# Performance work log

Hardware: AMD Instinct MI355X
Metric: run time of the kernel (lower is better)

## Reference

```python
import jax, jax.numpy as jnp
import numpy as np

N, E, MUL = 10000, 160000, 16
DIM = 9            # sum of 2l+1 for l=0..2
UV = 5             # 2*lmax+1
CONV = 9           # uv1 + uv2 - 1
ONE = CONV // 2 + 1
LOG2 = np.float32(np.log(2.0))


def _ssp(x):
    # ShiftedSoftPlus
    return jax.nn.softplus(x) - LOG2


def _build_a_w():
    # weight_align_matrix scaled by path_w ~ sqrt(2l+1): row l covers its (2l+1) block
    a = np.zeros((3, DIM), dtype=np.float32)
    off = 0
    for l in range(3):
        d = 2 * l + 1
        a[l, off:off + d] = np.sqrt(np.float32(d))
        off += d
    return jnp.asarray(a)


def setup_inputs() -> dict:
    key = jax.random.key(0)
    ks = jax.random.split(key, 14)
    inp = {
        "x": jax.random.normal(ks[0], (N, MUL, DIM), jnp.float32),
        "filter_sph": jax.random.normal(ks[1], (E, DIM), jnp.float32),
        "weight_in": jax.random.uniform(ks[2], (E, 8), jnp.float32),
        "edge_idx": jax.random.randint(ks[3], (2, E), 0, N),
        "Ux_re": jax.random.normal(ks[4], (DIM, UV, UV), jnp.float32),
        "Ux_im": jax.random.normal(ks[5], (DIM, UV, UV), jnp.float32),
        "Uf_re": jax.random.normal(ks[6], (DIM, UV, UV), jnp.float32),
        "Uf_im": jax.random.normal(ks[7], (DIM, UV, UV), jnp.float32),
        "Vout_re": jax.random.normal(ks[8], (CONV, ONE, DIM), jnp.float32),
        "Vout_im": jax.random.normal(ks[9], (CONV, ONE, DIM), jnp.float32),
        "W1": jax.random.normal(ks[10], (8, 64), jnp.float32),
        "W2": jax.random.normal(ks[11], (64, 64), jnp.float32),
        "W3": jax.random.normal(ks[12], (64, MUL * 3), jnp.float32),
        "a_w": _build_a_w(),
        "denominator": jnp.ones((1,), jnp.float32),
    }
    return inp


def _to_grid(coeff, U):
    # coeff [..., DIM] real; U [DIM, UV, UV] complex -> real grid [..., CONV, CONV]
    f = jnp.einsum('...d,duv->...uv', coeff.astype(U.dtype), U)
    pad = (CONV - UV) // 2
    cfg = [(0, 0)] * (f.ndim - 2) + [(pad, pad), (pad, pad)]
    fp = jnp.pad(f, cfg)
    fo = jnp.fft.ifftshift(fp, axes=(-2, -1))[..., :ONE]
    return jnp.fft.irfft2(fo, s=(CONV, CONV), axes=(-2, -1), norm='backward')


def reference(x, filter_sph, weight_in, edge_idx, Ux_re, Ux_im, Uf_re, Uf_im,
              Vout_re, Vout_im, W1, W2, W3, a_w, denominator):
    Ux = jax.lax.complex(Ux_re, Ux_im)
    Uf = jax.lax.complex(Uf_re, Uf_im)
    Vo = jax.lax.complex(Vout_re, Vout_im)
    edge_src = edge_idx[1]
    edge_dst = edge_idx[0]

    # node and filter signals on the CONVxCONV Fourier grid
    xf = _to_grid(x, Ux)                             # [N, MUL, 9, 9]
    yf = _to_grid(filter_sph[:, None, :], Uf)        # [E, 1, 9, 9]

    conv = xf[edge_src] * yf                         # [E, MUL, 9, 9]
    out_f = jnp.fft.rfft2(conv, axes=(-2, -1))       # [E, MUL, 9, 5] complex
    msg = jnp.einsum('emuv,uvd->emd', out_f, Vo).real  # ToSphericalBasis (hermitian input)

    # weight MLP (e3nn FullyConnectedNet: x @ W / sqrt(fan_in), ssp between)
    h = _ssp(weight_in @ W1 * (1.0 / np.sqrt(8.0, dtype=np.float32)))
    h = _ssp(h @ W2 * (1.0 / np.sqrt(64.0, dtype=np.float32)))
    w = (h @ W3 * (1.0 / np.sqrt(64.0, dtype=np.float32))).reshape(-1, MUL, 3)

    factor = jnp.einsum('emp,pd->emd', w, a_w)       # weight @ a_w
    message = msg * factor                           # [E, MUL, 9]

    out = jax.ops.segment_sum(message, edge_dst, num_segments=N)  # scatter-reduce sum
    return out / denominator[0]
```

## Files before the change

### kernel.cpp

```cpp
#include <hip/hip_runtime.h>
#include <math.h>

#define PI9 (2.0f * 3.14159265358979323846f / 9.0f)

typedef float f32x4 __attribute__((ext_vector_type(4)));
typedef unsigned short us8 __attribute__((ext_vector_type(8)));
typedef __bf16 bf16x8 __attribute__((ext_vector_type(8)));
typedef unsigned int u32x4 __attribute__((ext_vector_type(4)));

__device__ __forceinline__ float ssp_f(float x) {
  const float ax = fabsf(x);
  const float t = __expf(-ax);
  return fmaxf(x, 0.f) + __logf(1.f + t) - 0.69314718f;
}

__device__ __forceinline__ unsigned short f2bf(float f) {
  unsigned int u = __float_as_uint(f);
  unsigned int r = (u + 0x7FFFu + ((u >> 16) & 1u)) >> 16;
  return (unsigned short)r;
}

__device__ __forceinline__ float bfLO(unsigned int u) {
  return __uint_as_float(u << 16);
}
__device__ __forceinline__ float bfHI(unsigned int u) {
  return __uint_as_float(u & 0xffff0000u);
}

__global__ __launch_bounds__(256) void wconv_kernel(
    const float* __restrict__ W1, const float* __restrict__ W2,
    const float* __restrict__ W3, const float* __restrict__ a_w,
    const float* __restrict__ den, float* __restrict__ W1s,
    unsigned short* __restrict__ W2T, unsigned short* __restrict__ W3T) {
  const int i = blockIdx.x * 256 + threadIdx.x;
  const float invden = 1.f / den[0];
  const float sc0 = a_w[0] * invden, sc1 = a_w[10] * invden, sc2 = a_w[22] * invden;
  const float rs8 = 0.35355339059327373f;
  if (i < 512) {
    W1s[i] = W1[i] * rs8;
  } else if (i < 4608) {
    const int ii = i - 512;
    const int k = ii >> 6, j = ii & 63;
    W2T[j * 64 + ((((k >> 3) ^ (j & 7)) << 3)) + (k & 7)] = f2bf(W2[ii] * 0.125f);
  } else if (i < 7680) {
    const int ii = i - 4608;
    const int k = ii / 48, j = ii % 48;
    const int jm = j % 3;
    const float s = (jm == 0) ? sc0 : ((jm == 1) ? sc1 : sc2);
    W3T[j * 64 + ((((k >> 3) ^ (j & 7)) << 3)) + (k & 7)] = f2bf(W3[ii] * 0.125f * s);
  }
}

__device__ void precompute_body(
    int d, unsigned char* smem,
    const float* __restrict__ Ux_re, const float* __restrict__ Ux_im,
    const float* __restrict__ Uf_re, const float* __restrict__ Uf_im,
    const float* __restrict__ Vo_re, const float* __restrict__ Vo_im,
    float* __restrict__ CT) {
  float* G = (float*)smem;
  float* TL = (float*)(smem + 5840);
  float* cs9 = (float*)(smem + 8768);
  float* sn9 = (float*)(smem + 8816);
  const int t0 = threadIdx.x;

  if (t0 < 9) {
    float s, c;
    __sincosf(PI9 * (float)t0, &s, &c);
    cs9[t0] = c; sn9[t0] = s;
  }
  __syncthreads();

  for (int t = t0; t < 1458; t += 256) {
    const int which = t / 729, idx = t % 729;
    const int p = idx / 81, ab = idx % 81, a = ab / 9, b = ab % 9;
    const float* Ure = which ? Uf_re : Ux_re;
    const float* Uim = which ? Uf_im : Ux_im;
    float g = 0.f;
#pragma unroll
    for (int v = 0; v < 3; ++v) {
      const int uc = v + 2;
      float hre = 0.f, him = 0.f;
#pragma unroll
      for (int ui = 0; ui < 5; ++ui) {
        const int u = (ui + 7) % 9;
        const float re = Ure[p * 25 + ui * 5 + uc];
        const float im = Uim[p * 25 + ui * 5 + uc];
        const int k = (u * a) % 9;
        const float c = cs9[k], s = sn9[k];
        hre += re * c - im * s;
        him += re * s + im * c;
      }
      hre *= (1.f / 9.f); him *= (1.f / 9.f);
      if (v == 0) {
        g += hre;
      } else {
        const int k = (v * b) % 9;
        g += 2.f * (hre * cs9[k] - him * sn9[k]);
      }
    }
    G[which * 729 + p * 81 + ab] = g * (1.f / 9.f);
  }
  __syncthreads();

  for (int t = t0; t < 729; t += 256) {
    const int ab = t / 9, dd = t % 9, a = ab / 9, b = ab % 9;
    float acc = 0.f;
    for (int u = 0; u < 9; ++u)
      for (int v = 0; v < 5; ++v) {
        const int k = (u * a + v * b) % 9;
        acc += Vo_re[u * 45 + v * 9 + dd] * cs9[k]
             + Vo_im[u * 45 + v * 9 + dd] * sn9[k];
      }
    TL[ab * 9 + dd] = acc;
  }
  __syncthreads();

  if (t0 < 108) {
    const int p = t0 / 12, q = t0 % 12;
    float acc = 0.f;
    if (q < 9) {
      for (int ab = 0; ab < 81; ++ab)
        acc += G[p * 81 + ab] * G[729 + q * 81 + ab] * TL[ab * 9 + d];
    }
    CT[(d * 9 + p) * 12 + q] = acc;
  }
}

__device__ void mlp_body(
    int mblk, unsigned char* smem, const float* __restrict__ win,
    const float* __restrict__ W1s, const unsigned short* __restrict__ W2T,
    const unsigned short* __restrict__ W3T,
    unsigned short* __restrict__ w48b) {
  unsigned short* H1 = (unsigned short*)smem;
  unsigned short* H2 = (unsigned short*)(smem + 8192);
  const int t = threadIdx.x;
  const int w = t >> 6, l = t & 63;
  const int er = l & 15, g = l >> 4;
  unsigned short* h1p = H1 + w * 1024;
  unsigned short* h2p = H2 + w * 1024;

#pragma unroll 1
  for (int rep = 0; rep < 2; ++rep) {
    const int e = mblk * 128 + rep * 64 + w * 16 + er;

    float in8[8];
    {
      const float4 A = *(const float4*)(win + (size_t)e * 8);
      const float4 B = *(const float4*)(win + (size_t)e * 8 + 4);
      in8[0] = A.x; in8[1] = A.y; in8[2] = A.z; in8[3] = A.w;
      in8[4] = B.x; in8[5] = B.y; in8[6] = B.z; in8[7] = B.w;
    }
    float h[16];
#pragma unroll
    for (int c = 0; c < 16; ++c) h[c] = 0.f;
#pragma unroll
    for (int k = 0; k < 8; ++k) {
      const float* wr = W1s + k * 64 + g * 16;
      const float4 w0 = *(const float4*)wr;
      const float4 w1 = *(const float4*)(wr + 4);
      const float4 w2 = *(const float4*)(wr + 8);
      const float4 w3 = *(const float4*)(wr + 12);
      const float ik = in8[k];
      h[0]  = fmaf(ik, w0.x, h[0]);  h[1]  = fmaf(ik, w0.y, h[1]);
      h[2]  = fmaf(ik, w0.z, h[2]);  h[3]  = fmaf(ik, w0.w, h[3]);
      h[4]  = fmaf(ik, w1.x, h[4]);  h[5]  = fmaf(ik, w1.y, h[5]);
      h[6]  = fmaf(ik, w1.z, h[6]);  h[7]  = fmaf(ik, w1.w, h[7]);
      h[8]  = fmaf(ik, w2.x, h[8]);  h[9]  = fmaf(ik, w2.y, h[9]);
      h[10] = fmaf(ik, w2.z, h[10]); h[11] = fmaf(ik, w2.w, h[11]);
      h[12] = fmaf(ik, w3.x, h[12]); h[13] = fmaf(ik, w3.y, h[13]);
      h[14] = fmaf(ik, w3.z, h[14]); h[15] = fmaf(ik, w3.w, h[15]);
    }
    us8 pk0, pk1;
#pragma unroll
    for (int jj = 0; jj < 8; ++jj) pk0[jj] = f2bf(ssp_f(h[jj]));
#pragma unroll
    for (int jj = 0; jj < 8; ++jj) pk1[jj] = f2bf(ssp_f(h[8 + jj]));
    *(us8*)&h1p[er * 64 + (((2 * g) ^ (er & 7)) << 3)] = pk0;
    *(us8*)&h1p[er * 64 + (((2 * g + 1) ^ (er & 7)) << 3)] = pk1;
    __builtin_amdgcn_wave_barrier();

    const us8 a0 = *(const us8*)&h1p[er * 64 + ((g ^ (er & 7)) << 3)];
    const us8 a1 = *(const us8*)&h1p[er * 64 + (((g + 4) ^ (er & 7)) << 3)];
    float hh[16];
#pragma unroll
    for (int nt = 0; nt < 4; ++nt) {
      const int j = nt * 16 + er;
      const us8 b0 = *(const us8*)&W2T[j * 64 + ((g ^ (j & 7)) << 3)];
      const us8 b1 = *(const us8*)&W2T[j * 64 + (((g + 4) ^ (j & 7)) << 3)];
      f32x4 acc = {0.f, 0.f, 0.f, 0.f};
      acc = __builtin_amdgcn_mfma_f32_16x16x32_bf16(
          __builtin_bit_cast(bf16x8, a0), __builtin_bit_cast(bf16x8, b0), acc, 0, 0, 0);
      acc = __builtin_amdgcn_mfma_f32_16x16x32_bf16(
          __builtin_bit_cast(bf16x8, a1), __builtin_bit_cast(bf16x8, b1), acc, 0, 0, 0);
#pragma unroll
      for (int r = 0; r < 4; ++r) hh[nt * 4 + r] = ssp_f(acc[r]);
    }
#pragma unroll
    for (int nt = 0; nt < 4; ++nt)
#pragma unroll
      for (int r = 0; r < 4; ++r) {
        const int e2 = g * 4 + r;
        const int k2 = nt * 16 + er;
        h2p[e2 * 64 + ((((k2 >> 3) ^ (e2 & 7)) << 3)) + (k2 & 7)] = f2bf(hh[nt * 4 + r]);
      }
    __builtin_amdgcn_wave_barrier();

    const us8 c0 = *(const us8*)&h2p[er * 64 + ((g ^ (er & 7)) << 3)];
    const us8 c1 = *(const us8*)&h2p[er * 64 + (((g + 4) ^ (er & 7)) << 3)];
    const int ebase = mblk * 128 + rep * 64 + w * 16 + g * 4;
#pragma unroll
    for (int nt = 0; nt < 3; ++nt) {
      const int o = nt * 16 + er;
      const int om = o / 3, ol = o - om * 3;
      const us8 b0 = *(const us8*)&W3T[o * 64 + ((g ^ (o & 7)) << 3)];
      const us8 b1 = *(const us8*)&W3T[o * 64 + (((g + 4) ^ (o & 7)) << 3)];
      f32x4 acc = {0.f, 0.f, 0.f, 0.f};
      acc = __builtin_amdgcn_mfma_f32_16x16x32_bf16(
          __builtin_bit_cast(bf16x8, c0), __builtin_bit_cast(bf16x8, b0), acc, 0, 0, 0);
      acc = __builtin_amdgcn_mfma_f32_16x16x32_bf16(
          __builtin_bit_cast(bf16x8, c1), __builtin_bit_cast(bf16x8, b1), acc, 0, 0, 0);
#pragma unroll
      for (int r = 0; r < 4; ++r)
        w48b[(size_t)(ebase + r) * 64 + ol * 16 + om] = f2bf(acc[r]);
    }
    __builtin_amdgcn_wave_barrier();
  }
}

__global__ __launch_bounds__(256) void prep_kernel(
    const float* __restrict__ win, const float* __restrict__ W1s,
    const unsigned short* __restrict__ W2T,
    const unsigned short* __restrict__ W3T,
    unsigned short* __restrict__ w48b,
    const int* __restrict__ dst, const int* __restrict__ src, int E,
    int* __restrict__ cnt, int2* __restrict__ slots2,
    const float* __restrict__ xsrc, int NR, unsigned short* __restrict__ xbf,
    const float* __restrict__ Ux_re, const float* __restrict__ Ux_im,
    const float* __restrict__ Uf_re, const float* __restrict__ Uf_im,
    const float* __restrict__ Vo_re, const float* __restrict__ Vo_im,
    float* __restrict__ CT, int nScat, int nXc) {
  __shared__ __align__(16) unsigned char smem[16384];
  const int bid = blockIdx.x;
  if (bid < 9) {
    precompute_body(bid, smem, Ux_re, Ux_im, Uf_re, Uf_im, Vo_re, Vo_im, CT);
  } else if (bid < 9 + nScat) {
    const int e = (bid - 9) * 256 + threadIdx.x;
    if (e < E) {
      const int d = dst[e];
      const int pos = atomicAdd(&cnt[d], 1);
      if (pos < 96) slots2[(size_t)d * 96 + pos] = make_int2(e, src[e]);
    }
  } else if (bid < 9 + nScat + nXc) {
    const int r = (bid - 9 - nScat) * 256 + threadIdx.x;
    if (r < NR) {
      const float* xp = xsrc + (size_t)r * 9;
      unsigned int u0 = (unsigned)f2bf(xp[0]) | ((unsigned)f2bf(xp[1]) << 16);
      unsigned int u1 = (unsigned)f2bf(xp[2]) | ((unsigned)f2bf(xp[3]) << 16);
      unsigned int u2 = (unsigned)f2bf(xp[4]) | ((unsigned)f2bf(xp[5]) << 16);
      unsigned int u3 = (unsigned)f2bf(xp[6]) | ((unsigned)f2bf(xp[7]) << 16);
      unsigned int u4 = (unsigned)f2bf(xp[8]);
      unsigned short* op = xbf + (size_t)r * 12;
      *(uint2*)op = make_uint2(u0, u1);
      *(uint2*)(op + 4) = make_uint2(u2, u3);
      *(uint2*)(op + 8) = make_uint2(u4, 0u);
    }
  } else {
    mlp_body(bid - 9 - nScat - nXc, smem, win, W1s, W2T, W3T, w48b);
  }
}

__global__ __launch_bounds__(256) void node_kernel(
    const unsigned short* __restrict__ xbf, const float* __restrict__ filt,
    const int* __restrict__ cnt, const int2* __restrict__ slots2,
    const unsigned short* __restrict__ w48b, const float* __restrict__ CT,
    float* __restrict__ out, int N) {
  __shared__ __align__(16) unsigned short meL[4][2304];
  const int t = threadIdx.x, w = t >> 6, l = t & 63;
  const int n16 = l & 15, g = l >> 4;
  const int Ld = (n16 == 0) ? 0 : ((n16 < 4) ? 1 : 2);
  const bool dok = n16 < 9;
  const int drow = dok ? n16 : 0;
  const bool isg0 = (g == 0), isg1 = (g == 1);
  const int n = blockIdx.x * 4 + w;
  if (n >= N) return;

  int dT0, pT0, dT1, pT1, dT2, pT2, dT3, pT3, dT4, pT4, dT5, pT5;
  bool ok0, ok1, ok2, ok3, ok4, ok5;
  bf16x8 Bme0, Bme1, Bme2, Bme3, Bme4, Bme5;
#define MKB(tt, Bv, dv, pv, okv)                                             \
  {                                                                          \
    const int col = tt * 16 + n16;                                           \
    okv = (col < 81);                                                        \
    dv = okv ? col / 9 : 0;                                                  \
    pv = okv ? col % 9 : 0;                                                  \
    bf16x8 bv;                                                               \
    _Pragma("unroll")                                                        \
    for (int j = 0; j < 8; ++j) bv[j] = (__bf16)0.f;                         \
    if (okv) {                                                               \
      const float* cp = CT + col * 12;                                       \
      if (g == 0) {                                                          \
        const float4 ca = *(const float4*)cp;                                \
        const float4 cb = *(const float4*)(cp + 4);                          \
        bv[0] = (__bf16)ca.x; bv[1] = (__bf16)ca.y;                          \
        bv[2] = (__bf16)ca.z; bv[3] = (__bf16)ca.w;                          \
        bv[4] = (__bf16)cb.x; bv[5] = (__bf16)cb.y;                          \
        bv[6] = (__bf16)cb.z; bv[7] = (__bf16)cb.w;                          \
      } else if (g == 1) {                                                   \
        bv[0] = (__bf16)cp[8];                                               \
      }                                                                      \
    }                                                                        \
    Bv = bv;                                                                 \
  }
  MKB(0, Bme0, dT0, pT0, ok0); MKB(1, Bme1, dT1, pT1, ok1);
  MKB(2, Bme2, dT2, pT2, ok2); MKB(3, Bme3, dT3, pT3, ok3);
  MKB(4, Bme4, dT4, pT4, ok4); MKB(5, Bme5, dT5, pT5, ok5);
#undef MKB

  int deg = cnt[n];
  if (deg > 96) deg = 96;
  const int2* sl2 = slots2 + (size_t)n * 96;
  unsigned short* mlw = &meL[w][0];

  f32x4 accm = {0.f, 0.f, 0.f, 0.f};

  const int nb = (deg + 15) >> 4;
  for (int b = 0; b < nb; ++b) {
    const int base = b * 16;
    const int degb = (deg - base < 16) ? (deg - base) : 16;

    int esx = 0, esy = 0;
    if (n16 < degb) {
      const int2 v = sl2[base + n16];
      esx = v.x; esy = v.y;
    }
    bf16x8 Af;
#pragma unroll
    for (int j = 0; j < 8; ++j) Af[j] = (__bf16)0.f;
    if (n16 < degb) {
      const float* fp = filt + (size_t)esx * 9;
      if (g == 0) {
        const float4 fa = *(const float4*)fp;
        const float4 fb = *(const float4*)(fp + 4);
        Af[0] = (__bf16)fa.x; Af[1] = (__bf16)fa.y;
        Af[2] = (__bf16)fa.z; Af[3] = (__bf16)fa.w;
        Af[4] = (__bf16)fb.x; Af[5] = (__bf16)fb.y;
        Af[6] = (__bf16)fb.z; Af[7] = (__bf16)fb.w;
      } else if (g == 1) {
        Af[0] = (__bf16)fp[8];
      }
    }

#define MEMFMA(Bv, dv, pv, okv)                                              \
    {                                                                        \
      f32x4 a6 = {0.f, 0.f, 0.f, 0.f};                                       \
      a6 = __builtin_amdgcn_mfma_f32_16x16x32_bf16(Af, Bv, a6, 0, 0, 0);     \
      if (okv) {                                                             \
        _Pragma("unroll")                                                    \
        for (int r = 0; r < 4; ++r)                                          \
          mlw[(g * 4 + r) * 144 + dv * 16 + pv] = f2bf(a6[r]);               \
      }                                                                      \
    }
    MEMFMA(Bme0, dT0, pT0, ok0); MEMFMA(Bme1, dT1, pT1, ok1);
    MEMFMA(Bme2, dT2, pT2, ok2); MEMFMA(Bme3, dT3, pT3, ok3);
    MEMFMA(Bme4, dT4, pT4, ok4); MEMFMA(Bme5, dT5, pT5, ok5);
#undef MEMFMA
    __builtin_amdgcn_wave_barrier();

    for (int il = 0; il < degb; ++il) {
      const int e = __builtin_amdgcn_readlane(esx, il);
      const int s = __builtin_amdgcn_readlane(esy, il);

      const unsigned short* xrp = xbf + (size_t)s * 192 + n16 * 12;
      const u32x4 q = *(const u32x4*)xrp;
      const unsigned int qc = *(const unsigned int*)(xrp + 8);

      const uint2 wv =
          *(const uint2*)(w48b + (size_t)e * 64 + Ld * 16 + g * 4);

      const unsigned short* mr = mlw + il * 144 + drow * 16;
      const u32x4 mdv = *(const u32x4*)mr;
      const unsigned int md4 = (*(const unsigned int*)(mr + 8)) & 0xffffu;

      u32x4 av;
      av[0] = isg0 ? q[0] : (isg1 ? qc : 0u);
      av[1] = isg0 ? q[1] : 0u;
      av[2] = isg0 ? q[2] : 0u;
      av[3] = isg0 ? q[3] : 0u;
      u32x4 bv;
      bv[0] = isg0 ? mdv[0] : (isg1 ? md4 : 0u);
      bv[1] = isg0 ? mdv[1] : 0u;
      bv[2] = isg0 ? mdv[2] : 0u;
      bv[3] = isg0 ? mdv[3] : 0u;

      f32x4 c1 = {0.f, 0.f, 0.f, 0.f};
      c1 = __builtin_amdgcn_mfma_f32_16x16x32_bf16(
          __builtin_bit_cast(bf16x8, av), __builtin_bit_cast(bf16x8, bv),
          c1, 0, 0, 0);
      accm[0] = fmaf(c1[0], bfLO(wv.x), accm[0]);
      accm[1] = fmaf(c1[1], bfHI(wv.x), accm[1]);
      accm[2] = fmaf(c1[2], bfLO(wv.y), accm[2]);
      accm[3] = fmaf(c1[3], bfHI(wv.y), accm[3]);
    }
    __builtin_amdgcn_wave_barrier();
  }

  if (dok) {
    float* op = out + (size_t)n * 144 + (g * 4) * 9 + n16;
    op[0]  = accm[0];
    op[9]  = accm[1];
    op[18] = accm[2];
    op[27] = accm[3];
  }
}

extern "C" void kernel_launch(void* const* d_in, const int* in_sizes, int n_in,
                              void* d_out, int out_size, void* d_ws, size_t ws_size,
                              hipStream_t stream) {
  const float* x      = (const float*)d_in[0];
  const float* filt   = (const float*)d_in[1];
  const float* win    = (const float*)d_in[2];
  const int*   eidx   = (const int*)d_in[3];
  const float* Ux_re  = (const float*)d_in[4];
  const float* Ux_im  = (const float*)d_in[5];
  const float* Uf_re  = (const float*)d_in[6];
  const float* Uf_im  = (const float*)d_in[7];
  const float* Vo_re  = (const float*)d_in[8];
  const float* Vo_im  = (const float*)d_in[9];
  const float* W1     = (const float*)d_in[10];
  const float* W2     = (const float*)d_in[11];
  const float* W3     = (const float*)d_in[12];
  const float* a_w    = (const float*)d_in[13];
  const float* den    = (const float*)d_in[14];
  float* out = (float*)d_out;

  const int N = in_sizes[0] / 144;
  const int E = in_sizes[3] / 2;
  const int NR = N * 16;
  const int* dst = eidx;
  const int* src = eidx + E;

  char* wsb = (char*)d_ws;
  const size_t off_cnt  = 8192;
  const size_t off_slot = off_cnt + 40960;
  const size_t off_w48  = off_slot + (size_t)N * 96 * 8;
  const size_t off_xbf  = off_w48 + (size_t)E * 64 * 2;
  const size_t off_w1s  = off_xbf + (size_t)NR * 12 * 2;
  const size_t off_w2t  = off_w1s + 512 * 4;
  const size_t off_w3t  = off_w2t + 4096 * 2;

  float*          CT    = (float*)wsb;
  int*            cnt   = (int*)(wsb + off_cnt);
  int2*           slot2 = (int2*)(wsb + off_slot);
  unsigned short* w48b  = (unsigned short*)(wsb + off_w48);
  unsigned short* xbf   = (unsigned short*)(wsb + off_xbf);
  float*          W1s   = (float*)(wsb + off_w1s);
  unsigned short* W2T   = (unsigned short*)(wsb + off_w2t);
  unsigned short* W3T   = (unsigned short*)(wsb + off_w3t);

  const int nMlp  = E / 128;
  const int nScat = (E + 255) / 256;
  const int nXc   = (NR + 255) / 256;

  hipMemsetAsync(cnt, 0, (size_t)N * sizeof(int), stream);
  wconv_kernel<<<30, 256, 0, stream>>>(W1, W2, W3, a_w, den, W1s, W2T, W3T);
  prep_kernel<<<9 + nScat + nXc + nMlp, 256, 0, stream>>>(
      win, W1s, W2T, W3T, w48b,
      dst, src, E, cnt, slot2,
      x, NR, xbf,
      Ux_re, Ux_im, Uf_re, Uf_im, Vo_re, Vo_im, CT, nScat, nXc);
  node_kernel<<<(N + 3) / 4, 256, 0, stream>>>(
      xbf, filt, cnt, slot2, w48b, CT, out, N);
}
```

Measured before the change: 88.99 us.

## Fuse per-edge weight MLP into node kernel and fold count memset into wconv

Moves the per-edge MLP (W1/W2/W3 with ssp) out of prep_kernel and computes it inside node_kernel for each batch of 16 incoming edges. The resulting weights stay in LDS instead of going through a global w48b buffer. The count array is zeroed inside wconv_kernel instead of by a separate memset, so one launch is dropped. This removes the E×64 bf16 write and the gathered read-back, and shrinks prep_kernel. In exchange, the MLP work moves into the latency-critical node kernel and now runs per destination node, where partial edge batches lead to uneven utilisation. wconv_kernel also grows to cover N threads.

```diff
diff --git a/kernel.cpp b/kernel.cpp
--- a/kernel.cpp
+++ b/kernel.cpp
@@ -31,11 +31,13 @@
     const float* __restrict__ W1, const float* __restrict__ W2,
     const float* __restrict__ W3, const float* __restrict__ a_w,
     const float* __restrict__ den, float* __restrict__ W1s,
-    unsigned short* __restrict__ W2T, unsigned short* __restrict__ W3T) {
+    unsigned short* __restrict__ W2T, unsigned short* __restrict__ W3T,
+    int* __restrict__ cnt, int N) {
   const int i = blockIdx.x * 256 + threadIdx.x;
   const float invden = 1.f / den[0];
   const float sc0 = a_w[0] * invden, sc1 = a_w[10] * invden, sc2 = a_w[22] * invden;
   const float rs8 = 0.35355339059327373f;
+  if (i < N) cnt[i] = 0;
   if (i < 512) {
     W1s[i] = W1[i] * rs8;
   } else if (i < 4608) {
@@ -126,120 +128,15 @@
   }
 }
 
-__device__ void mlp_body(
-    int mblk, unsigned char* smem, const float* __restrict__ win,
-    const float* __restrict__ W1s, const unsigned short* __restrict__ W2T,
-    const unsigned short* __restrict__ W3T,
-    unsigned short* __restrict__ w48b) {
-  unsigned short* H1 = (unsigned short*)smem;
-  unsigned short* H2 = (unsigned short*)(smem + 8192);
-  const int t = threadIdx.x;
-  const int w = t >> 6, l = t & 63;
-  const int er = l & 15, g = l >> 4;
-  unsigned short* h1p = H1 + w * 1024;
-  unsigned short* h2p = H2 + w * 1024;
-
-#pragma unroll 1
-  for (int rep = 0; rep < 2; ++rep) {
-    const int e = mblk * 128 + rep * 64 + w * 16 + er;
-
-    float in8[8];
-    {
-      const float4 A = *(const float4*)(win + (size_t)e * 8);
-      const float4 B = *(const float4*)(win + (size_t)e * 8 + 4);
-      in8[0] = A.x; in8[1] = A.y; in8[2] = A.z; in8[3] = A.w;
-      in8[4] = B.x; in8[5] = B.y; in8[6] = B.z; in8[7] = B.w;
-    }
-    float h[16];
-#pragma unroll
-    for (int c = 0; c < 16; ++c) h[c] = 0.f;
-#pragma unroll
-    for (int k = 0; k < 8; ++k) {
-      const float* wr = W1s + k * 64 + g * 16;
-      const float4 w0 = *(const float4*)wr;
-      const float4 w1 = *(const float4*)(wr + 4);
-      const float4 w2 = *(const float4*)(wr + 8);
-      const float4 w3 = *(const float4*)(wr + 12);
-      const float ik = in8[k];
-      h[0]  = fmaf(ik, w0.x, h[0]);  h[1]  = fmaf(ik, w0.y, h[1]);
-      h[2]  = fmaf(ik, w0.z, h[2]);  h[3]  = fmaf(ik, w0.w, h[3]);
-      h[4]  = fmaf(ik, w1.x, h[4]);  h[5]  = fmaf(ik, w1.y, h[5]);
-      h[6]  = fmaf(ik, w1.z, h[6]);  h[7]  = fmaf(ik, w1.w, h[7]);
-      h[8]  = fmaf(ik, w2.x, h[8]);  h[9]  = fmaf(ik, w2.y, h[9]);
-      h[10] = fmaf(ik, w2.z, h[10]); h[11] = fmaf(ik, w2.w, h[11]);
-      h[12] = fmaf(ik, w3.x, h[12]); h[13] = fmaf(ik, w3.y, h[13]);
-      h[14] = fmaf(ik, w3.z, h[14]); h[15] = fmaf(ik, w3.w, h[15]);
-    }
-    us8 pk0, pk1;
-#pragma unroll
-    for (int jj = 0; jj < 8; ++jj) pk0[jj] = f2bf(ssp_f(h[jj]));
-#pragma unroll
-    for (int jj = 0; jj < 8; ++jj) pk1[jj] = f2bf(ssp_f(h[8 + jj]));
-    *(us8*)&h1p[er * 64 + (((2 * g) ^ (er & 7)) << 3)] = pk0;
-    *(us8*)&h1p[er * 64 + (((2 * g + 1) ^ (er & 7)) << 3)] = pk1;
-    __builtin_amdgcn_wave_barrier();
-
-    const us8 a0 = *(const us8*)&h1p[er * 64 + ((g ^ (er & 7)) << 3)];
-    const us8 a1 = *(const us8*)&h1p[er * 64 + (((g + 4) ^ (er & 7)) << 3)];
-    float hh[16];
-#pragma unroll
-    for (int nt = 0; nt < 4; ++nt) {
-      const int j = nt * 16 + er;
-      const us8 b0 = *(const us8*)&W2T[j * 64 + ((g ^ (j & 7)) << 3)];
-      const us8 b1 = *(const us8*)&W2T[j * 64 + (((g + 4) ^ (j & 7)) << 3)];
-      f32x4 acc = {0.f, 0.f, 0.f, 0.f};
-      acc = __builtin_amdgcn_mfma_f32_16x16x32_bf16(
-          __builtin_bit_cast(bf16x8, a0), __builtin_bit_cast(bf16x8, b0), acc, 0, 0, 0);
-      acc = __builtin_amdgcn_mfma_f32_16x16x32_bf16(
-          __builtin_bit_cast(bf16x8, a1), __builtin_bit_cast(bf16x8, b1), acc, 0, 0, 0);
-#pragma unroll
-      for (int r = 0; r < 4; ++r) hh[nt * 4 + r] = ssp_f(acc[r]);
-    }
-#pragma unroll
-    for (int nt = 0; nt < 4; ++nt)
-#pragma unroll
-      for (int r = 0; r < 4; ++r) {
-        const int e2 = g * 4 + r;
-        const int k2 = nt * 16 + er;
-        h2p[e2 * 64 + ((((k2 >> 3) ^ (e2 & 7)) << 3)) + (k2 & 7)] = f2bf(hh[nt * 4 + r]);
-      }
-    __builtin_amdgcn_wave_barrier();
-
-    const us8 c0 = *(const us8*)&h2p[er * 64 + ((g ^ (er & 7)) << 3)];
-    const us8 c1 = *(const us8*)&h2p[er * 64 + (((g + 4) ^ (er & 7)) << 3)];
-    const int ebase = mblk * 128 + rep * 64 + w * 16 + g * 4;
-#pragma unroll
-    for (int nt = 0; nt < 3; ++nt) {
-      const int o = nt * 16 + er;
-      const int om = o / 3, ol = o - om * 3;
-      const us8 b0 = *(const us8*)&W3T[o * 64 + ((g ^ (o & 7)) << 3)];
-      const us8 b1 = *(const us8*)&W3T[o * 64 + (((g + 4) ^ (o & 7)) << 3)];
-      f32x4 acc = {0.f, 0.f, 0.f, 0.f};
-      acc = __builtin_amdgcn_mfma_f32_16x16x32_bf16(
-          __builtin_bit_cast(bf16x8, c0), __builtin_bit_cast(bf16x8, b0), acc, 0, 0, 0);
-      acc = __builtin_amdgcn_mfma_f32_16x16x32_bf16(
-          __builtin_bit_cast(bf16x8, c1), __builtin_bit_cast(bf16x8, b1), acc, 0, 0, 0);
-#pragma unroll
-      for (int r = 0; r < 4; ++r)
-        w48b[(size_t)(ebase + r) * 64 + ol * 16 + om] = f2bf(acc[r]);
-    }
-    __builtin_amdgcn_wave_barrier();
-  }
-}
-
 __global__ __launch_bounds__(256) void prep_kernel(
-    const float* __restrict__ win, const float* __restrict__ W1s,
-    const unsigned short* __restrict__ W2T,
-    const unsigned short* __restrict__ W3T,
-    unsigned short* __restrict__ w48b,
     const int* __restrict__ dst, const int* __restrict__ src, int E,
     int* __restrict__ cnt, int2* __restrict__ slots2,
     const float* __restrict__ xsrc, int NR, unsigned short* __restrict__ xbf,
     const float* __restrict__ Ux_re, const float* __restrict__ Ux_im,
     const float* __restrict__ Uf_re, const float* __restrict__ Uf_im,
     const float* __restrict__ Vo_re, const float* __restrict__ Vo_im,
-    float* __restrict__ CT, int nScat, int nXc) {
-  __shared__ __align__(16) unsigned char smem[16384];
+    float* __restrict__ CT, int nScat) {
+  __shared__ __align__(16) unsigned char smem[9216];
   const int bid = blockIdx.x;
   if (bid < 9) {
     precompute_body(bid, smem, Ux_re, Ux_im, Uf_re, Uf_im, Vo_re, Vo_im, CT);
@@ -250,7 +147,7 @@
       const int pos = atomicAdd(&cnt[d], 1);
       if (pos < 96) slots2[(size_t)d * 96 + pos] = make_int2(e, src[e]);
     }
-  } else if (bid < 9 + nScat + nXc) {
+  } else {
     const int r = (bid - 9 - nScat) * 256 + threadIdx.x;
     if (r < NR) {
       const float* xp = xsrc + (size_t)r * 9;
@@ -264,17 +161,17 @@
       *(uint2*)(op + 4) = make_uint2(u2, u3);
       *(uint2*)(op + 8) = make_uint2(u4, 0u);
     }
-  } else {
-    mlp_body(bid - 9 - nScat - nXc, smem, win, W1s, W2T, W3T, w48b);
   }
 }
 
 __global__ __launch_bounds__(256) void node_kernel(
     const unsigned short* __restrict__ xbf, const float* __restrict__ filt,
+    const float* __restrict__ win, const float* __restrict__ W1s,
+    const unsigned short* __restrict__ W2T,
+    const unsigned short* __restrict__ W3T,
     const int* __restrict__ cnt, const int2* __restrict__ slots2,
-    const unsigned short* __restrict__ w48b, const float* __restrict__ CT,
-    float* __restrict__ out, int N) {
-  __shared__ __align__(16) unsigned short meL[4][2304];
+    const float* __restrict__ CT, float* __restrict__ out, int N) {
+  __shared__ __align__(16) unsigned short BUF[4][3072];
   const int t = threadIdx.x, w = t >> 6, l = t & 63;
   const int n16 = l & 15, g = l >> 4;
   const int Ld = (n16 == 0) ? 0 : ((n16 < 4) ? 1 : 2);
@@ -283,6 +180,12 @@
   const bool isg0 = (g == 0), isg1 = (g == 1);
   const int n = blockIdx.x * 4 + w;
   if (n >= N) return;
+
+  unsigned short* bw = &BUF[w][0];
+  unsigned short* H1 = bw;
+  unsigned short* H2 = bw + 1024;
+  unsigned short* meL = bw;
+  unsigned short* w48L = bw + 2304;
 
   int dT0, pT0, dT1, pT1, dT2, pT2, dT3, pT3, dT4, pT4, dT5, pT5;
   bool ok0, ok1, ok2, ok3, ok4, ok5;
@@ -319,7 +222,6 @@
   int deg = cnt[n];
   if (deg > 96) deg = 96;
   const int2* sl2 = slots2 + (size_t)n * 96;
-  unsigned short* mlw = &meL[w][0];
 
   f32x4 accm = {0.f, 0.f, 0.f, 0.f};
 
@@ -333,6 +235,9 @@
       const int2 v = sl2[base + n16];
       esx = v.x; esy = v.y;
     }
+    const float* wp = win + (size_t)esx * 8;
+    const float4 wa4 = *(const float4*)wp;
+    const float4 wb4 = *(const float4*)(wp + 4);
     bf16x8 Af;
 #pragma unroll
     for (int j = 0; j < 8; ++j) Af[j] = (__bf16)0.f;
@@ -350,6 +255,89 @@
       }
     }
 
+    if (b) __builtin_amdgcn_wave_barrier();
+
+    {
+      float in8[8] = {wa4.x, wa4.y, wa4.z, wa4.w, wb4.x, wb4.y, wb4.z, wb4.w};
+      float h[16];
+#pragma unroll
+      for (int c = 0; c < 16; ++c) h[c] = 0.f;
+#pragma unroll
+      for (int k = 0; k < 8; ++k) {
+        const float* wr = W1s + k * 64 + g * 16;
+        const float4 w0 = *(const float4*)wr;
+        const float4 w1 = *(const float4*)(wr + 4);
+        const float4 w2 = *(const float4*)(wr + 8);
+        const float4 w3 = *(const float4*)(wr + 12);
+        const float ik = in8[k];
+        h[0]  = fmaf(ik, w0.x, h[0]);  h[1]  = fmaf(ik, w0.y, h[1]);
+        h[2]  = fmaf(ik, w0.z, h[2]);  h[3]  = fmaf(ik, w0.w, h[3]);
+        h[4]  = fmaf(ik, w1.x, h[4]);  h[5]  = fmaf(ik, w1.y, h[5]);
+        h[6]  = fmaf(ik, w1.z, h[6]);  h[7]  = fmaf(ik, w1.w, h[7]);
+        h[8]  = fmaf(ik, w2.x, h[8]);  h[9]  = fmaf(ik, w2.y, h[9]);
+        h[10] = fmaf(ik, w2.z, h[10]); h[11] = fmaf(ik, w2.w, h[11]);
+        h[12] = fmaf(ik, w3.x, h[12]); h[13] = fmaf(ik, w3.y, h[13]);
+        h[14] = fmaf(ik, w3.z, h[14]); h[15] = fmaf(ik, w3.w, h[15]);
+      }
+      us8 pk0, pk1;
+#pragma unroll
+      for (int jj = 0; jj < 8; ++jj) pk0[jj] = f2bf(ssp_f(h[jj]));
+#pragma unroll
+      for (int jj = 0; jj < 8; ++jj) pk1[jj] = f2bf(ssp_f(h[8 + jj]));
+      *(us8*)&H1[n16 * 64 + (((2 * g) ^ (n16 & 7)) << 3)] = pk0;
+      *(us8*)&H1[n16 * 64 + (((2 * g + 1) ^ (n16 & 7)) << 3)] = pk1;
+    }
+    __builtin_amdgcn_wave_barrier();
+
+    {
+      const us8 a0 = *(const us8*)&H1[n16 * 64 + ((g ^ (n16 & 7)) << 3)];
+      const us8 a1 = *(const us8*)&H1[n16 * 64 + (((g + 4) ^ (n16 & 7)) << 3)];
+      float hh[16];
+#pragma unroll
+      for (int nt = 0; nt < 4; ++nt) {
+        const int j = nt * 16 + n16;
+        const us8 b0 = *(const us8*)&W2T[j * 64 + ((g ^ (j & 7)) << 3)];
+        const us8 b1 = *(const us8*)&W2T[j * 64 + (((g + 4) ^ (j & 7)) << 3)];
+        f32x4 acc = {0.f, 0.f, 0.f, 0.f};
+        acc = __builtin_amdgcn_mfma_f32_16x16x32_bf16(
+            __builtin_bit_cast(bf16x8, a0), __builtin_bit_cast(bf16x8, b0), acc, 0, 0, 0);
+        acc = __builtin_amdgcn_mfma_f32_16x16x32_bf16(
+            __builtin_bit_cast(bf16x8, a1), __builtin_bit_cast(bf16x8, b1), acc, 0, 0, 0);
+#pragma unroll
+        for (int r = 0; r < 4; ++r) hh[nt * 4 + r] = ssp_f(acc[r]);
+      }
+#pragma unroll
+      for (int nt = 0; nt < 4; ++nt)
+#pragma unroll
+        for (int r = 0; r < 4; ++r) {
+          const int e2 = g * 4 + r;
+          const int k2 = nt * 16 + n16;
+          H2[e2 * 64 + ((((k2 >> 3) ^ (e2 & 7)) << 3)) + (k2 & 7)] = f2bf(hh[nt * 4 + r]);
+        }
+    }
+    __builtin_amdgcn_wave_barrier();
+
+    {
+      const us8 c0 = *(const us8*)&H2[n16 * 64 + ((g ^ (n16 & 7)) << 3)];
+      const us8 c1 = *(const us8*)&H2[n16 * 64 + (((g + 4) ^ (n16 & 7)) << 3)];
+#pragma unroll
+      for (int nt = 0; nt < 3; ++nt) {
+        const int o = nt * 16 + n16;
+        const int om = o / 3, ol = o - om * 3;
+        const us8 b0 = *(const us8*)&W3T[o * 64 + ((g ^ (o & 7)) << 3)];
+        const us8 b1 = *(const us8*)&W3T[o * 64 + (((g + 4) ^ (o & 7)) << 3)];
+        f32x4 acc = {0.f, 0.f, 0.f, 0.f};
+        acc = __builtin_amdgcn_mfma_f32_16x16x32_bf16(
+            __builtin_bit_cast(bf16x8, c0), __builtin_bit_cast(bf16x8, b0), acc, 0, 0, 0);
+        acc = __builtin_amdgcn_mfma_f32_16x16x32_bf16(
+            __builtin_bit_cast(bf16x8, c1), __builtin_bit_cast(bf16x8, b1), acc, 0, 0, 0);
+#pragma unroll
+        for (int r = 0; r < 4; ++r)
+          w48L[(g * 4 + r) * 48 + ol * 16 + om] = f2bf(acc[r]);
+      }
+    }
+    __builtin_amdgcn_wave_barrier();
+
 #define MEMFMA(Bv, dv, pv, okv)                                              \
     {                                                                        \
       f32x4 a6 = {0.f, 0.f, 0.f, 0.f};                                       \
@@ -357,7 +345,7 @@
       if (okv) {                                                             \
         _Pragma("unroll")                                                    \
         for (int r = 0; r < 4; ++r)                                          \
-          mlw[(g * 4 + r) * 144 + dv * 16 + pv] = f2bf(a6[r]);               \
+          meL[(g * 4 + r) * 144 + dv * 16 + pv] = f2bf(a6[r]);               \
       }                                                                      \
     }
     MEMFMA(Bme0, dT0, pT0, ok0); MEMFMA(Bme1, dT1, pT1, ok1);
@@ -367,17 +355,15 @@
     __builtin_amdgcn_wave_barrier();
 
     for (int il = 0; il < degb; ++il) {
-      const int e = __builtin_amdgcn_readlane(esx, il);
       const int s = __builtin_amdgcn_readlane(esy, il);
 
       const unsigned short* xrp = xbf + (size_t)s * 192 + n16 * 12;
       const u32x4 q = *(const u32x4*)xrp;
       const unsigned int qc = *(const unsigned int*)(xrp + 8);
 
-      const uint2 wv =
-          *(const uint2*)(w48b + (size_t)e * 64 + Ld * 16 + g * 4);
-
-      const unsigned short* mr = mlw + il * 144 + drow * 16;
+      const uint2 wv = *(const uint2*)(w48L + il * 48 + Ld * 16 + g * 4);
+
+      const unsigned short* mr = meL + il * 144 + drow * 16;
       const u32x4 mdv = *(const u32x4*)mr;
       const unsigned int md4 = (*(const unsigned int*)(mr + 8)) & 0xffffu;
 
@@ -401,7 +387,6 @@
       accm[2] = fmaf(c1[2], bfLO(wv.y), accm[2]);
       accm[3] = fmaf(c1[3], bfHI(wv.y), accm[3]);
     }
-    __builtin_amdgcn_wave_barrier();
   }
 
   if (dok) {
@@ -442,8 +427,7 @@
   char* wsb = (char*)d_ws;
   const size_t off_cnt  = 8192;
   const size_t off_slot = off_cnt + 40960;
-  const size_t off_w48  = off_slot + (size_t)N * 96 * 8;
-  const size_t off_xbf  = off_w48 + (size_t)E * 64 * 2;
+  const size_t off_xbf  = off_slot + (size_t)N * 96 * 8;
   const size_t off_w1s  = off_xbf + (size_t)NR * 12 * 2;
   const size_t off_w2t  = off_w1s + 512 * 4;
   const size_t off_w3t  = off_w2t + 4096 * 2;
@@ -451,23 +435,20 @@
   float*          CT    = (float*)wsb;
   int*            cnt   = (int*)(wsb + off_cnt);
   int2*           slot2 = (int2*)(wsb + off_slot);
-  unsigned short* w48b  = (unsigned short*)(wsb + off_w48);
   unsigned short* xbf   = (unsigned short*)(wsb + off_xbf);
   float*          W1s   = (float*)(wsb + off_w1s);
   unsigned short* W2T   = (unsigned short*)(wsb + off_w2t);
   unsigned short* W3T   = (unsigned short*)(wsb + off_w3t);
 
-  const int nMlp  = E / 128;
   const int nScat = (E + 255) / 256;
   const int nXc   = (NR + 255) / 256;
 
-  hipMemsetAsync(cnt, 0, (size_t)N * sizeof(int), stream);
-  wconv_kernel<<<30, 256, 0, stream>>>(W1, W2, W3, a_w, den, W1s, W2T, W3T);
-  prep_kernel<<<9 + nScat + nXc + nMlp, 256, 0, stream>>>(
-      win, W1s, W2T, W3T, w48b,
+  wconv_kernel<<<(N + 255) / 256, 256, 0, stream>>>(
+      W1, W2, W3, a_w, den, W1s, W2T, W3T, cnt, N);
+  prep_kernel<<<9 + nScat + nXc, 256, 0, stream>>>(
       dst, src, E, cnt, slot2,
       x, NR, xbf,
-      Ux_re, Ux_im, Uf_re, Uf_im, Vo_re, Vo_im, CT, nScat, nXc);
+      Ux_re, Ux_im, Uf_re, Uf_im, Vo_re, Vo_im, CT, nScat);
   node_kernel<<<(N + 3) / 4, 256, 0, stream>>>(
-      xbf, filt, cnt, slot2, w48b, CT, out, N);
-}
+      xbf, filt, win, W1s, W2T, W3T, cnt, slot2, CT, out, N);
+}
```

New measurement: 215.8 us. 143% more time.

## Split MLP into own kernel, use MFMA for first layer, fold memset into wconv

Applied to the files above, without the earlier changes.

The weight MLP moves out of the fused prep kernel into a dedicated kernel. Its first layer now runs on bf16 MFMA with a transposed bf16 W1, replacing per-lane FMA loops. The count memset is folded into the weight-conversion kernel, whose grid grows to cover N. This adds a kernel launch and lowers first-layer precision to bf16 inputs. In exchange it shrinks the heterogeneous prep kernel's LDS footprint and removes VALU work.

```diff
diff --git a/kernel.cpp b/kernel.cpp
--- a/kernel.cpp
+++ b/kernel.cpp
@@ -30,14 +30,17 @@
 __global__ __launch_bounds__(256) void wconv_kernel(
     const float* __restrict__ W1, const float* __restrict__ W2,
     const float* __restrict__ W3, const float* __restrict__ a_w,
-    const float* __restrict__ den, float* __restrict__ W1s,
-    unsigned short* __restrict__ W2T, unsigned short* __restrict__ W3T) {
+    const float* __restrict__ den, unsigned short* __restrict__ W1T,
+    unsigned short* __restrict__ W2T, unsigned short* __restrict__ W3T,
+    int* __restrict__ cnt, int N) {
   const int i = blockIdx.x * 256 + threadIdx.x;
   const float invden = 1.f / den[0];
   const float sc0 = a_w[0] * invden, sc1 = a_w[10] * invden, sc2 = a_w[22] * invden;
   const float rs8 = 0.35355339059327373f;
+  if (i < N) cnt[i] = 0;
   if (i < 512) {
-    W1s[i] = W1[i] * rs8;
+    const int col = i & 63, kk = i >> 6;
+    W1T[col * 8 + kk] = f2bf(W1[kk * 64 + col] * rs8);
   } else if (i < 4608) {
     const int ii = i - 512;
     const int k = ii >> 6, j = ii & 63;
@@ -126,120 +129,15 @@
   }
 }
 
-__device__ void mlp_body(
-    int mblk, unsigned char* smem, const float* __restrict__ win,
-    const float* __restrict__ W1s, const unsigned short* __restrict__ W2T,
-    const unsigned short* __restrict__ W3T,
-    unsigned short* __restrict__ w48b) {
-  unsigned short* H1 = (unsigned short*)smem;
-  unsigned short* H2 = (unsigned short*)(smem + 8192);
-  const int t = threadIdx.x;
-  const int w = t >> 6, l = t & 63;
-  const int er = l & 15, g = l >> 4;
-  unsigned short* h1p = H1 + w * 1024;
-  unsigned short* h2p = H2 + w * 1024;
-
-#pragma unroll 1
-  for (int rep = 0; rep < 2; ++rep) {
-    const int e = mblk * 128 + rep * 64 + w * 16 + er;
-
-    float in8[8];
-    {
-      const float4 A = *(const float4*)(win + (size_t)e * 8);
-      const float4 B = *(const float4*)(win + (size_t)e * 8 + 4);
-      in8[0] = A.x; in8[1] = A.y; in8[2] = A.z; in8[3] = A.w;
-      in8[4] = B.x; in8[5] = B.y; in8[6] = B.z; in8[7] = B.w;
-    }
-    float h[16];
-#pragma unroll
-    for (int c = 0; c < 16; ++c) h[c] = 0.f;
-#pragma unroll
-    for (int k = 0; k < 8; ++k) {
-      const float* wr = W1s + k * 64 + g * 16;
-      const float4 w0 = *(const float4*)wr;
-      const float4 w1 = *(const float4*)(wr + 4);
-      const float4 w2 = *(const float4*)(wr + 8);
-      const float4 w3 = *(const float4*)(wr + 12);
-      const float ik = in8[k];
-      h[0]  = fmaf(ik, w0.x, h[0]);  h[1]  = fmaf(ik, w0.y, h[1]);
-      h[2]  = fmaf(ik, w0.z, h[2]);  h[3]  = fmaf(ik, w0.w, h[3]);
-      h[4]  = fmaf(ik, w1.x, h[4]);  h[5]  = fmaf(ik, w1.y, h[5]);
-      h[6]  = fmaf(ik, w1.z, h[6]);  h[7]  = fmaf(ik, w1.w, h[7]);
-      h[8]  = fmaf(ik, w2.x, h[8]);  h[9]  = fmaf(ik, w2.y, h[9]);
-      h[10] = fmaf(ik, w2.z, h[10]); h[11] = fmaf(ik, w2.w, h[11]);
-      h[12] = fmaf(ik, w3.x, h[12]); h[13] = fmaf(ik, w3.y, h[13]);
-      h[14] = fmaf(ik, w3.z, h[14]); h[15] = fmaf(ik, w3.w, h[15]);
-    }
-    us8 pk0, pk1;
-#pragma unroll
-    for (int jj = 0; jj < 8; ++jj) pk0[jj] = f2bf(ssp_f(h[jj]));
-#pragma unroll
-    for (int jj = 0; jj < 8; ++jj) pk1[jj] = f2bf(ssp_f(h[8 + jj]));
-    *(us8*)&h1p[er * 64 + (((2 * g) ^ (er & 7)) << 3)] = pk0;
-    *(us8*)&h1p[er * 64 + (((2 * g + 1) ^ (er & 7)) << 3)] = pk1;
-    __builtin_amdgcn_wave_barrier();
-
-    const us8 a0 = *(const us8*)&h1p[er * 64 + ((g ^ (er & 7)) << 3)];
-    const us8 a1 = *(const us8*)&h1p[er * 64 + (((g + 4) ^ (er & 7)) << 3)];
-    float hh[16];
-#pragma unroll
-    for (int nt = 0; nt < 4; ++nt) {
-      const int j = nt * 16 + er;
-      const us8 b0 = *(const us8*)&W2T[j * 64 + ((g ^ (j & 7)) << 3)];
-      const us8 b1 = *(const us8*)&W2T[j * 64 + (((g + 4) ^ (j & 7)) << 3)];
-      f32x4 acc = {0.f, 0.f, 0.f, 0.f};
-      acc = __builtin_amdgcn_mfma_f32_16x16x32_bf16(
-          __builtin_bit_cast(bf16x8, a0), __builtin_bit_cast(bf16x8, b0), acc, 0, 0, 0);
-      acc = __builtin_amdgcn_mfma_f32_16x16x32_bf16(
-          __builtin_bit_cast(bf16x8, a1), __builtin_bit_cast(bf16x8, b1), acc, 0, 0, 0);
-#pragma unroll
-      for (int r = 0; r < 4; ++r) hh[nt * 4 + r] = ssp_f(acc[r]);
-    }
-#pragma unroll
-    for (int nt = 0; nt < 4; ++nt)
-#pragma unroll
-      for (int r = 0; r < 4; ++r) {
-        const int e2 = g * 4 + r;
-        const int k2 = nt * 16 + er;
-        h2p[e2 * 64 + ((((k2 >> 3) ^ (e2 & 7)) << 3)) + (k2 & 7)] = f2bf(hh[nt * 4 + r]);
-      }
-    __builtin_amdgcn_wave_barrier();
-
-    const us8 c0 = *(const us8*)&h2p[er * 64 + ((g ^ (er & 7)) << 3)];
-    const us8 c1 = *(const us8*)&h2p[er * 64 + (((g + 4) ^ (er & 7)) << 3)];
-    const int ebase = mblk * 128 + rep * 64 + w * 16 + g * 4;
-#pragma unroll
-    for (int nt = 0; nt < 3; ++nt) {
-      const int o = nt * 16 + er;
-      const int om = o / 3, ol = o - om * 3;
-      const us8 b0 = *(const us8*)&W3T[o * 64 + ((g ^ (o & 7)) << 3)];
-      const us8 b1 = *(const us8*)&W3T[o * 64 + (((g + 4) ^ (o & 7)) << 3)];
-      f32x4 acc = {0.f, 0.f, 0.f, 0.f};
-      acc = __builtin_amdgcn_mfma_f32_16x16x32_bf16(
-          __builtin_bit_cast(bf16x8, c0), __builtin_bit_cast(bf16x8, b0), acc, 0, 0, 0);
-      acc = __builtin_amdgcn_mfma_f32_16x16x32_bf16(
-          __builtin_bit_cast(bf16x8, c1), __builtin_bit_cast(bf16x8, b1), acc, 0, 0, 0);
-#pragma unroll
-      for (int r = 0; r < 4; ++r)
-        w48b[(size_t)(ebase + r) * 64 + ol * 16 + om] = f2bf(acc[r]);
-    }
-    __builtin_amdgcn_wave_barrier();
-  }
-}
-
-__global__ __launch_bounds__(256) void prep_kernel(
-    const float* __restrict__ win, const float* __restrict__ W1s,
-    const unsigned short* __restrict__ W2T,
-    const unsigned short* __restrict__ W3T,
-    unsigned short* __restrict__ w48b,
+__global__ __launch_bounds__(256) void prep_misc(
     const int* __restrict__ dst, const int* __restrict__ src, int E,
     int* __restrict__ cnt, int2* __restrict__ slots2,
     const float* __restrict__ xsrc, int NR, unsigned short* __restrict__ xbf,
     const float* __restrict__ Ux_re, const float* __restrict__ Ux_im,
     const float* __restrict__ Uf_re, const float* __restrict__ Uf_im,
     const float* __restrict__ Vo_re, const float* __restrict__ Vo_im,
-    float* __restrict__ CT, int nScat, int nXc) {
-  __shared__ __align__(16) unsigned char smem[16384];
+    float* __restrict__ CT, int nScat) {
+  __shared__ __align__(16) unsigned char smem[9216];
   const int bid = blockIdx.x;
   if (bid < 9) {
     precompute_body(bid, smem, Ux_re, Ux_im, Uf_re, Uf_im, Vo_re, Vo_im, CT);
@@ -250,7 +148,7 @@
       const int pos = atomicAdd(&cnt[d], 1);
       if (pos < 96) slots2[(size_t)d * 96 + pos] = make_int2(e, src[e]);
     }
-  } else if (bid < 9 + nScat + nXc) {
+  } else {
     const int r = (bid - 9 - nScat) * 256 + threadIdx.x;
     if (r < NR) {
       const float* xp = xsrc + (size_t)r * 9;
@@ -264,8 +162,108 @@
       *(uint2*)(op + 4) = make_uint2(u2, u3);
       *(uint2*)(op + 8) = make_uint2(u4, 0u);
     }
-  } else {
-    mlp_body(bid - 9 - nScat - nXc, smem, win, W1s, W2T, W3T, w48b);
+  }
+}
+
+__global__ __launch_bounds__(256) void mlp_kernel(
+    const float* __restrict__ win, const unsigned short* __restrict__ W1T,
+    const unsigned short* __restrict__ W2T,
+    const unsigned short* __restrict__ W3T,
+    unsigned short* __restrict__ w48b, int E) {
+  __shared__ __align__(16) unsigned short H1[4][1024];
+  __shared__ __align__(16) unsigned short H2[4][1024];
+  const int t = threadIdx.x;
+  const int w = t >> 6, l = t & 63;
+  const int n16 = l & 15, g = l >> 4;
+  unsigned short* h1p = &H1[w][0];
+  unsigned short* h2p = &H2[w][0];
+  const bool isg0 = (g == 0);
+
+#pragma unroll 1
+  for (int rep = 0; rep < 2; ++rep) {
+    const int e = blockIdx.x * 128 + rep * 64 + w * 16 + n16;
+
+    bf16x8 Aw;
+#pragma unroll
+    for (int j = 0; j < 8; ++j) Aw[j] = (__bf16)0.f;
+    if (isg0) {
+      const float4 A = *(const float4*)(win + (size_t)e * 8);
+      const float4 B = *(const float4*)(win + (size_t)e * 8 + 4);
+      Aw[0] = (__bf16)A.x; Aw[1] = (__bf16)A.y;
+      Aw[2] = (__bf16)A.z; Aw[3] = (__bf16)A.w;
+      Aw[4] = (__bf16)B.x; Aw[5] = (__bf16)B.y;
+      Aw[6] = (__bf16)B.z; Aw[7] = (__bf16)B.w;
+    }
+#pragma unroll
+    for (int nt = 0; nt < 4; ++nt) {
+      const int col = nt * 16 + n16;
+      us8 bz;
+#pragma unroll
+      for (int j = 0; j < 8; ++j) bz[j] = 0;
+      const us8 bw = isg0 ? *(const us8*)&W1T[col * 8] : bz;
+      f32x4 acc = {0.f, 0.f, 0.f, 0.f};
+      acc = __builtin_amdgcn_mfma_f32_16x16x32_bf16(
+          Aw, __builtin_bit_cast(bf16x8, bw), acc, 0, 0, 0);
+#pragma unroll
+      for (int r = 0; r < 4; ++r) {
+        const int e2 = g * 4 + r;
+        const int k2 = nt * 16 + n16;
+        h1p[e2 * 64 + ((((k2 >> 3) ^ (e2 & 7)) << 3)) + (k2 & 7)] =
+            f2bf(ssp_f(acc[r]));
+      }
+    }
+    __builtin_amdgcn_wave_barrier();
+
+    {
+      const us8 a0 = *(const us8*)&h1p[n16 * 64 + ((g ^ (n16 & 7)) << 3)];
+      const us8 a1 = *(const us8*)&h1p[n16 * 64 + (((g + 4) ^ (n16 & 7)) << 3)];
+      float hh[16];
+#pragma unroll
+      for (int nt = 0; nt < 4; ++nt) {
+        const int j = nt * 16 + n16;
+        const us8 b0 = *(const us8*)&W2T[j * 64 + ((g ^ (j & 7)) << 3)];
+        const us8 b1 = *(const us8*)&W2T[j * 64 + (((g + 4) ^ (j & 7)) << 3)];
+        f32x4 acc = {0.f, 0.f, 0.f, 0.f};
+        acc = __builtin_amdgcn_mfma_f32_16x16x32_bf16(
+            __builtin_bit_cast(bf16x8, a0), __builtin_bit_cast(bf16x8, b0), acc, 0, 0, 0);
+        acc = __builtin_amdgcn_mfma_f32_16x16x32_bf16(
+            __builtin_bit_cast(bf16x8, a1), __builtin_bit_cast(bf16x8, b1), acc, 0, 0, 0);
+#pragma unroll
+        for (int r = 0; r < 4; ++r) hh[nt * 4 + r] = ssp_f(acc[r]);
+      }
+#pragma unroll
+      for (int nt = 0; nt < 4; ++nt)
+#pragma unroll
+        for (int r = 0; r < 4; ++r) {
+          const int e2 = g * 4 + r;
+          const int k2 = nt * 16 + n16;
+          h2p[e2 * 64 + ((((k2 >> 3) ^ (e2 & 7)) << 3)) + (k2 & 7)] =
+              f2bf(hh[nt * 4 + r]);
+        }
+    }
+    __builtin_amdgcn_wave_barrier();
+
+    {
+      const us8 c0 = *(const us8*)&h2p[n16 * 64 + ((g ^ (n16 & 7)) << 3)];
+      const us8 c1 = *(const us8*)&h2p[n16 * 64 + (((g + 4) ^ (n16 & 7)) << 3)];
+      const int ebase = blockIdx.x * 128 + rep * 64 + w * 16 + g * 4;
+#pragma unroll
+      for (int nt = 0; nt < 3; ++nt) {
+        const int o = nt * 16 + n16;
+        const int om = o / 3, ol = o - om * 3;
+        const us8 b0 = *(const us8*)&W3T[o * 64 + ((g ^ (o & 7)) << 3)];
+        const us8 b1 = *(const us8*)&W3T[o * 64 + (((g + 4) ^ (o & 7)) << 3)];
+        f32x4 acc = {0.f, 0.f, 0.f, 0.f};
+        acc = __builtin_amdgcn_mfma_f32_16x16x32_bf16(
+            __builtin_bit_cast(bf16x8, c0), __builtin_bit_cast(bf16x8, b0), acc, 0, 0, 0);
+        acc = __builtin_amdgcn_mfma_f32_16x16x32_bf16(
+            __builtin_bit_cast(bf16x8, c1), __builtin_bit_cast(bf16x8, b1), acc, 0, 0, 0);
+#pragma unroll
+        for (int r = 0; r < 4; ++r)
+          w48b[(size_t)(ebase + r) * 64 + ol * 16 + om] = f2bf(acc[r]);
+      }
+    }
+    __builtin_amdgcn_wave_barrier();
   }
 }
 
@@ -444,8 +442,8 @@
   const size_t off_slot = off_cnt + 40960;
   const size_t off_w48  = off_slot + (size_t)N * 96 * 8;
   const size_t off_xbf  = off_w48 + (size_t)E * 64 * 2;
-  const size_t off_w1s  = off_xbf + (size_t)NR * 12 * 2;
-  const size_t off_w2t  = off_w1s + 512 * 4;
+  const size_t off_w1t  = off_xbf + (size_t)NR * 12 * 2;
+  const size_t off_w2t  = off_w1t + 512 * 2;
   const size_t off_w3t  = off_w2t + 4096 * 2;
 
   float*          CT    = (float*)wsb;
@@ -453,21 +451,21 @@
   int2*           slot2 = (int2*)(wsb + off_slot);
   unsigned short* w48b  = (unsigned short*)(wsb + off_w48);
   unsigned short* xbf   = (unsigned short*)(wsb + off_xbf);
-  float*          W1s   = (float*)(wsb + off_w1s);
+  unsigned short* W1T   = (unsigned short*)(wsb + off_w1t);
   unsigned short* W2T   = (unsigned short*)(wsb + off_w2t);
   unsigned short* W3T   = (unsigned short*)(wsb + off_w3t);
 
-  const int nMlp  = E / 128;
   const int nScat = (E + 255) / 256;
   const int nXc   = (NR + 255) / 256;
-
-  hipMemsetAsync(cnt, 0, (size_t)N * sizeof(int), stream);
-  wconv_kernel<<<30, 256, 0, stream>>>(W1, W2, W3, a_w, den, W1s, W2T, W3T);
-  prep_kernel<<<9 + nScat + nXc + nMlp, 256, 0, stream>>>(
-      win, W1s, W2T, W3T, w48b,
+  const int nMlp  = E / 128;
+
+  wconv_kernel<<<(N + 255) / 256, 256, 0, stream>>>(
+      W1, W2, W3, a_w, den, W1T, W2T, W3T, cnt, N);
+  prep_misc<<<9 + nScat + nXc, 256, 0, stream>>>(
       dst, src, E, cnt, slot2,
       x, NR, xbf,
-      Ux_re, Ux_im, Uf_re, Uf_im, Vo_re, Vo_im, CT, nScat, nXc);
+      Ux_re, Ux_im, Uf_re, Uf_im, Vo_re, Vo_im, CT, nScat);
+  mlp_kernel<<<nMlp, 256, 0, stream>>>(win, W1T, W2T, W3T, w48b, E);
   node_kernel<<<(N + 3) / 4, 256, 0, stream>>>(
       xbf, filt, cnt, slot2, w48b, CT, out, N);
 }
```

Result: slower. 94.17 us (+5.8%).
